# Kernel tuning notes

Measured on AMD Instinct MI355X. Metric: run time of the kernel, lower is better.

Reference implementation:

```python
import jax, jax.numpy as jnp
import numpy as np

HID = 1024      # hidden_size (embedding dim, GRU input)
RNN = 1024      # rnn_hidden_size
VOCAB = 50000   # max_node
STEPS = 1024    # num_steps
SOS = 0


def setup_inputs() -> dict:
    key = jax.random.key(0)
    ks = jax.random.split(key, 8)
    s = 0.02
    return {
        "inputs": jax.random.randint(ks[0], (STEPS,), 0, VOCAB),
        "z": jax.random.normal(ks[1], (RNN,), jnp.float32),
        "emb_W": jax.random.uniform(ks[2], (VOCAB, HID), jnp.float32, -0.001, 0.001),
        "out_b": jnp.full((VOCAB,), 0.01, jnp.float32),
        "h2e_W": jax.random.normal(ks[3], (HID, RNN), jnp.float32) * s,
        "h2e_b": jnp.full((HID,), 0.01, jnp.float32),
        "W_ih": jax.random.normal(ks[4], (3 * RNN, HID), jnp.float32) * s,
        "W_hh": jax.random.normal(ks[5], (3 * RNN, RNN), jnp.float32) * s,
        "b_ih": jnp.zeros((3 * RNN,), jnp.float32),
        "b_hh": jnp.zeros((3 * RNN,), jnp.float32),
    }


def reference(inputs, z, emb_W, out_b, h2e_W, h2e_b, W_ih, W_hh, b_ih, b_hh):
    R = RNN

    def gru_cell(h, x):
        gi = W_ih @ x + b_ih          # (3R,)
        gh = W_hh @ h + b_hh          # (3R,)
        r = jax.nn.sigmoid(gi[:R] + gh[:R])
        zg = jax.nn.sigmoid(gi[R:2 * R] + gh[R:2 * R])
        n = jnp.tanh(gi[2 * R:] + r * gh[2 * R:])
        return (1.0 - zg) * n + zg * h

    # teacher forcing: step i consumes token_{i-1} (SOS for i=1), target is inputs[i]
    step_tokens = jnp.concatenate([jnp.array([SOS], dtype=inputs.dtype), inputs[1:-1]])
    targets = inputs[1:]

    def step(h, tok_tgt):
        tok, tgt = tok_tgt
        x = emb_W[tok]                              # embedding lookup (HID,)
        h_new = gru_cell(h, x)                      # (RNN,)
        e = h2e_W @ h_new + h2e_b                   # (HID,)
        logp = jax.nn.log_softmax(emb_W @ e + out_b)  # tied weights, (VOCAB,)
        return h_new, (-logp[tgt], jnp.argmax(logp))

    _, (losses, preds) = jax.lax.scan(step, z, (step_tokens, targets))
    loss = jnp.sum(losses)
    outputs = jnp.zeros((1, inputs.shape[0]), dtype=jnp.int32).at[0, 1:].set(preds.astype(jnp.int32))
    return loss, outputs
```

## Files before the change

kernel.cpp:

```cpp
#include <hip/hip_runtime.h>
#include <math.h>

#define NV      50000
#define T_STEPS 1023
#define KDIM    1024
#define NCH     782
typedef unsigned long long ull;


__global__ __launch_bounds__(256) void k_gather(const int* __restrict__ inputs,
                                                const float* __restrict__ emb,
                                                float* __restrict__ X) {
  const int t = blockIdx.x;
  const int tid = threadIdx.x;
  float4 v = make_float4(0.f, 0.f, 0.f, 0.f);
  if (t < T_STEPS) {
    const int tok = (t == 0) ? 0 : inputs[t];
    v = *(const float4*)&emb[(size_t)tok * KDIM + tid * 4];
  }
  *(float4*)&X[(size_t)t * KDIM + tid * 4] = v;
}

__global__ __launch_bounds__(256) void k_gemm_ffd(const float* __restrict__ A,
                                                  const float* __restrict__ B,
                                                  const float* __restrict__ bias,
                                                  double* __restrict__ C,
                                                  int N, int K) {
  __shared__ float As[32][68];
  __shared__ float Bs[32][68];
  const int tid = threadIdx.x;
  const int bx = blockIdx.x, by = blockIdx.y;
  const int lr = tid >> 2;
  const int lk = (tid & 3) * 8;
  const float* Ap = A + (size_t)(by * 64 + lr) * K + lk;
  const float* Bp = B + (size_t)(bx * 64 + lr) * K + lk;
  const int r0 = (tid >> 4) * 4;
  const int c0 = (tid & 15) * 4;
  double acc[4][4] = {};
  for (int kc = 0; kc < K; kc += 32) {
    const float4 a0 = *(const float4*)(Ap + kc);
    const float4 a1 = *(const float4*)(Ap + kc + 4);
    const float4 b0 = *(const float4*)(Bp + kc);
    const float4 b1 = *(const float4*)(Bp + kc + 4);
    __syncthreads();
    As[lk+0][lr]=a0.x; As[lk+1][lr]=a0.y; As[lk+2][lr]=a0.z; As[lk+3][lr]=a0.w;
    As[lk+4][lr]=a1.x; As[lk+5][lr]=a1.y; As[lk+6][lr]=a1.z; As[lk+7][lr]=a1.w;
    Bs[lk+0][lr]=b0.x; Bs[lk+1][lr]=b0.y; Bs[lk+2][lr]=b0.z; Bs[lk+3][lr]=b0.w;
    Bs[lk+4][lr]=b1.x; Bs[lk+5][lr]=b1.y; Bs[lk+6][lr]=b1.z; Bs[lk+7][lr]=b1.w;
    __syncthreads();
#pragma unroll
    for (int kk = 0; kk < 32; ++kk) {
      const float4 av = *(const float4*)&As[kk][r0];
      const float4 bv = *(const float4*)&Bs[kk][c0];
      const double aa[4] = {av.x, av.y, av.z, av.w};
      const double bb[4] = {bv.x, bv.y, bv.z, bv.w};
#pragma unroll
      for (int i = 0; i < 4; ++i)
#pragma unroll
        for (int j = 0; j < 4; ++j)
          acc[i][j] = fma(aa[i], bb[j], acc[i][j]);
    }
  }
  const int row = by * 64 + r0;
  const int col = bx * 64 + c0;
#pragma unroll
  for (int i = 0; i < 4; ++i)
#pragma unroll
    for (int j = 0; j < 4; ++j)
      C[(size_t)(row + i) * N + col + j] = acc[i][j] + (double)bias[col + j];
}

__global__ __launch_bounds__(256) void k_gemm_dfd(const double* __restrict__ A,
                                                  const float* __restrict__ B,
                                                  const float* __restrict__ bias,
                                                  double* __restrict__ C,
                                                  int N, int K) {
  __shared__ double As[32][68];
  __shared__ float  Bs[32][68];
  const int tid = threadIdx.x;
  const int bx = blockIdx.x, by = blockIdx.y;
  const int lr = tid >> 2;
  const int lk = (tid & 3) * 8;
  const double* Ap = A + (size_t)(by * 64 + lr) * K + lk;
  const float*  Bp = B + (size_t)(bx * 64 + lr) * K + lk;
  const int r0 = (tid >> 4) * 4;
  const int c0 = (tid & 15) * 4;
  double acc[4][4] = {};
  for (int kc = 0; kc < K; kc += 32) {
    double ar[8];
#pragma unroll
    for (int q = 0; q < 8; ++q) ar[q] = Ap[kc + q];
    const float4 b0 = *(const float4*)(Bp + kc);
    const float4 b1 = *(const float4*)(Bp + kc + 4);
    __syncthreads();
#pragma unroll
    for (int q = 0; q < 8; ++q) As[lk + q][lr] = ar[q];
    Bs[lk+0][lr]=b0.x; Bs[lk+1][lr]=b0.y; Bs[lk+2][lr]=b0.z; Bs[lk+3][lr]=b0.w;
    Bs[lk+4][lr]=b1.x; Bs[lk+5][lr]=b1.y; Bs[lk+6][lr]=b1.z; Bs[lk+7][lr]=b1.w;
    __syncthreads();
#pragma unroll
    for (int kk = 0; kk < 32; ++kk) {
      const double aa[4] = {As[kk][r0+0], As[kk][r0+1], As[kk][r0+2], As[kk][r0+3]};
      const float4 bv = *(const float4*)&Bs[kk][c0];
      const double bb[4] = {bv.x, bv.y, bv.z, bv.w};
#pragma unroll
      for (int i = 0; i < 4; ++i)
#pragma unroll
        for (int j = 0; j < 4; ++j)
          acc[i][j] = fma(aa[i], bb[j], acc[i][j]);
    }
  }
  const int row = by * 64 + r0;
  const int col = bx * 64 + c0;
#pragma unroll
  for (int i = 0; i < 4; ++i)
#pragma unroll
    for (int j = 0; j < 4; ++j)
      C[(size_t)(row + i) * N + col + j] = acc[i][j] + (double)bias[col + j];
}

__global__ __launch_bounds__(512, 2) void k_recur(const float* __restrict__ z,
                                                  const float* __restrict__ Whh,
                                                  const float* __restrict__ bhh,
                                                  const double* __restrict__ GI,
                                                  double* H, ull* SA, ull* SB,
                                                  int* done) {
  __shared__ double hs[1024];
  const int tid = threadIdx.x;
  const int w = tid >> 6, l = tid & 63;
  const int ibase = blockIdx.x * 16 + w * 2;
  float wreg[6][16];
#pragma unroll
  for (int il = 0; il < 2; ++il)
#pragma unroll
    for (int g = 0; g < 3; ++g) {
      const float* wp = Whh + (size_t)(g * 1024 + ibase + il) * 1024 + l;
#pragma unroll
      for (int m = 0; m < 16; ++m) wreg[il * 3 + g][m] = wp[m * 64];
    }
  double bh[6];
#pragma unroll
  for (int il = 0; il < 2; ++il)
#pragma unroll
    for (int g = 0; g < 3; ++g) bh[il * 3 + g] = (double)bhh[g * 1024 + ibase + il];

  hs[tid]       = (double)z[tid];
  hs[tid + 512] = (double)z[tid + 512];
  double gi[6];
#pragma unroll
  for (int il = 0; il < 2; ++il)
#pragma unroll
    for (int g = 0; g < 3; ++g) gi[il * 3 + g] = GI[g * 1024 + ibase + il];
  __syncthreads();

  for (int t = 0; t < T_STEPS; ++t) {
    const bool more = (t + 1 < T_STEPS);
    const int p = t & 1;
    const bool gate = more && (t >= 2);
    int dv = 0x7FFFFFFF;
    if (gate && tid < 64)
      dv = __hip_atomic_load(done + p * 64 + tid,
                             __ATOMIC_RELAXED, __HIP_MEMORY_SCOPE_AGENT);
    double s[6] = {0.0, 0.0, 0.0, 0.0, 0.0, 0.0};
#pragma unroll
    for (int m = 0; m < 16; ++m) {
      const double hv = hs[l + 64 * m];
#pragma unroll
      for (int rr = 0; rr < 6; ++rr) s[rr] = fma((double)wreg[rr][m], hv, s[rr]);
    }
#pragma unroll
    for (int rr = 0; rr < 6; ++rr) {
      double v = s[rr];
#pragma unroll
      for (int mk = 32; mk >= 1; mk >>= 1) v += __shfl_xor(v, mk, 64);
      s[rr] = v;
    }
    double hn = 0.0;
    if (l < 2) {
      const int il = l;
      const double r  = 1.0 / (1.0 + exp(-(gi[il * 3 + 0] + s[il * 3 + 0] + bh[il * 3 + 0])));
      const double zg = 1.0 / (1.0 + exp(-(gi[il * 3 + 1] + s[il * 3 + 1] + bh[il * 3 + 1])));
      const double n  = tanh(gi[il * 3 + 2] + r * (s[il * 3 + 2] + bh[il * 3 + 2]));
      hn = (1.0 - zg) * n + zg * hs[ibase + l];
    }
    double gin[6] = {0.0, 0.0, 0.0, 0.0, 0.0, 0.0};
    if (more) {
      const double* gp = GI + (size_t)(t + 1) * 3072;
#pragma unroll
      for (int il = 0; il < 2; ++il)
#pragma unroll
        for (int g = 0; g < 3; ++g) gin[il * 3 + g] = gp[g * 1024 + ibase + il];
    }
    if (gate && tid < 64) {
      while (!__all(dv >= t - 1)) {
        __builtin_amdgcn_s_sleep(1);
        dv = __hip_atomic_load(done + p * 64 + tid,
                               __ATOMIC_RELAXED, __HIP_MEMORY_SCOPE_AGENT);
      }
    }
    __syncthreads();
    if (l < 2) {
      const int gidx = ibase + l;
      __hip_atomic_store(H + (size_t)t * 1024 + gidx, hn,
                         __ATOMIC_RELAXED, __HIP_MEMORY_SCOPE_AGENT);
      if (more) {
        const ull hb  = (ull)__double_as_longlong(hn);
        const ull tag = ((ull)(t + 1)) << 32;
        __hip_atomic_store(SA + p * 1024 + gidx, tag | (hb >> 32),
                           __ATOMIC_RELAXED, __HIP_MEMORY_SCOPE_AGENT);
        __hip_atomic_store(SB + p * 1024 + gidx, tag | (hb & 0xFFFFFFFFull),
                           __ATOMIC_RELAXED, __HIP_MEMORY_SCOPE_AGENT);
      }
    }
    if (more) {
      const ull want = (ull)(t + 1);
      ull a0, b0, a1, b1;
      while (true) {
        a0 = __hip_atomic_load(SA + p * 1024 + tid,
                               __ATOMIC_RELAXED, __HIP_MEMORY_SCOPE_AGENT);
        b0 = __hip_atomic_load(SB + p * 1024 + tid,
                               __ATOMIC_RELAXED, __HIP_MEMORY_SCOPE_AGENT);
        if ((a0 >> 32) >= want && (b0 >> 32) >= want) break;
        __builtin_amdgcn_s_sleep(1);
      }
      while (true) {
        a1 = __hip_atomic_load(SA + p * 1024 + tid + 512,
                               __ATOMIC_RELAXED, __HIP_MEMORY_SCOPE_AGENT);
        b1 = __hip_atomic_load(SB + p * 1024 + tid + 512,
                               __ATOMIC_RELAXED, __HIP_MEMORY_SCOPE_AGENT);
        if ((a1 >> 32) >= want && (b1 >> 32) >= want) break;
        __builtin_amdgcn_s_sleep(1);
      }
      hs[tid]       = __longlong_as_double((long long)
                        (((a0 & 0xFFFFFFFFull) << 32) | (b0 & 0xFFFFFFFFull)));
      hs[tid + 512] = __longlong_as_double((long long)
                        (((a1 & 0xFFFFFFFFull) << 32) | (b1 & 0xFFFFFFFFull)));
      __syncthreads();
      if (tid == 0)
        __hip_atomic_store(done + p * 64 + blockIdx.x, t + 1,
                           __ATOMIC_RELAXED, __HIP_MEMORY_SCOPE_AGENT);
#pragma unroll
      for (int q = 0; q < 6; ++q) gi[q] = gin[q];
    }
  }
}

__global__ __launch_bounds__(256) void k_logits(const double* __restrict__ E,
                                                const float* __restrict__ emb,
                                                const float* __restrict__ out_b,
                                                const int* __restrict__ inputs,
                                                float* __restrict__ candL,
                                                int* __restrict__ candI,
                                                float* __restrict__ Psum,
                                                float* __restrict__ Ttgt) {
  __shared__ double As[32][68];
  __shared__ float  Bs[32][68];
  const int tid = threadIdx.x;
  const int bx = blockIdx.x, by = blockIdx.y;
  const int lr = tid >> 2;
  const int lk = (tid & 3) * 8;
  const int brow = bx * 64 + lr;
  const double* Ap = E + (size_t)(by * 64 + lr) * KDIM + lk;
  const float*  Bp = emb + (size_t)brow * KDIM + lk;
  const bool bvalid = (brow < NV);
  const int r0 = (tid >> 4) * 4;
  const int c0 = (tid & 15) * 4;
  double acc[4][4] = {};
  for (int kc = 0; kc < KDIM; kc += 32) {
    double ar[8];
#pragma unroll
    for (int q = 0; q < 8; ++q) ar[q] = Ap[kc + q];
    float4 b0 = make_float4(0.f, 0.f, 0.f, 0.f);
    float4 b1 = make_float4(0.f, 0.f, 0.f, 0.f);
    if (bvalid) { b0 = *(const float4*)(Bp + kc); b1 = *(const float4*)(Bp + kc + 4); }
    __syncthreads();
#pragma unroll
    for (int q = 0; q < 8; ++q) As[lk + q][lr] = ar[q];
    Bs[lk+0][lr]=b0.x; Bs[lk+1][lr]=b0.y; Bs[lk+2][lr]=b0.z; Bs[lk+3][lr]=b0.w;
    Bs[lk+4][lr]=b1.x; Bs[lk+5][lr]=b1.y; Bs[lk+6][lr]=b1.z; Bs[lk+7][lr]=b1.w;
    __syncthreads();
#pragma unroll
    for (int kk = 0; kk < 32; ++kk) {
      const double aa[4] = {As[kk][r0+0], As[kk][r0+1], As[kk][r0+2], As[kk][r0+3]};
      const float4 bv = *(const float4*)&Bs[kk][c0];
      const double bb[4] = {bv.x, bv.y, bv.z, bv.w};
#pragma unroll
      for (int i = 0; i < 4; ++i)
#pragma unroll
        for (int j = 0; j < 4; ++j)
          acc[i][j] = fma(aa[i], bb[j], acc[i][j]);
    }
  }
  const int colb = bx * 64 + c0;
#pragma unroll
  for (int i = 0; i < 4; ++i) {
    const int s = by * 64 + r0 + i;
    const bool valid = (s < T_STEPS);
    const int tgt = valid ? inputs[s + 1] : -1;
    float L1 = -3e38f, L2 = -3e38f;
    int   i1 = 0x7FFFFFFF, i2 = 0x7FFFFFFF;
    float se = 0.f, tv = -INFINITY;
#pragma unroll
    for (int j = 0; j < 4; ++j) {
      const int v = colb + j;
      if (v < NV) {
        const double lgd = acc[i][j] + (double)out_b[v];
        const float L = (float)lgd;
        se += expf((float)(lgd - 0.01));
        if (v == tgt) tv = (float)lgd;
        if (L > L1 || (L == L1 && v < i1)) { L2 = L1; i2 = i1; L1 = L; i1 = v; }
        else if (L > L2 || (L == L2 && v < i2)) { L2 = L; i2 = v; }
      }
    }
#pragma unroll
    for (int mk = 1; mk <= 8; mk <<= 1) {
      const float oL1 = __shfl_xor(L1, mk, 64); const int oi1 = __shfl_xor(i1, mk, 64);
      const float oL2 = __shfl_xor(L2, mk, 64); const int oi2 = __shfl_xor(i2, mk, 64);
      if (oL1 > L1 || (oL1 == L1 && oi1 < i1)) { L2 = L1; i2 = i1; L1 = oL1; i1 = oi1; }
      else if (oL1 > L2 || (oL1 == L2 && oi1 < i2)) { L2 = oL1; i2 = oi1; }
      if (oL2 > L1 || (oL2 == L1 && oi2 < i1)) { L2 = L1; i2 = i1; L1 = oL2; i1 = oi2; }
      else if (oL2 > L2 || (oL2 == L2 && oi2 < i2)) { L2 = oL2; i2 = oi2; }
      se += __shfl_xor(se, mk, 64);
      tv = fmaxf(tv, __shfl_xor(tv, mk, 64));
    }
    if (((tid & 15) == 0) && valid) {
      const size_t p = (size_t)s * (2 * NCH) + 2 * bx;
      candL[p] = L1;     candI[p] = i1;
      candL[p + 1] = L2; candI[p + 1] = i2;
      atomicAdd(&Psum[s], se);
      if (tv > -1e30f) Ttgt[s] = tv;
    }
  }
}

__global__ __launch_bounds__(256) void k_preds(const float* __restrict__ candL,
                                               const int* __restrict__ candI,
                                               float* __restrict__ out) {
  __shared__ float sL[256];
  __shared__ int   sI[256];
  const int s = blockIdx.x;
  const int tid = threadIdx.x;
  const int n = 2 * NCH;
  const size_t base = (size_t)s * n;
  float m = -3e38f;
  for (int c = tid; c < n; c += 256) m = fmaxf(m, candL[base + c]);
  sL[tid] = m; __syncthreads();
  for (int st = 128; st > 0; st >>= 1) {
    if (tid < st) sL[tid] = fmaxf(sL[tid], sL[tid + st]);
    __syncthreads();
  }
  const float Lmax = sL[0];
  __syncthreads();
  float bq = -3e38f; int bi = 0x7FFFFFFF;
  for (int c = tid; c < n; c += 256) {
    const float L = candL[base + c];
    const int   v = candI[base + c];
    const float d = L - Lmax;
    const float q = d - 10.8125f;
    if (q > bq || (q == bq && v < bi)) { bq = q; bi = v; }
  }
  sL[tid] = bq; sI[tid] = bi; __syncthreads();
  for (int st = 128; st > 0; st >>= 1) {
    if (tid < st) {
      if (sL[tid + st] > sL[tid] ||
          (sL[tid + st] == sL[tid] && sI[tid + st] < sI[tid])) {
        sL[tid] = sL[tid + st]; sI[tid] = sI[tid + st];
      }
    }
    __syncthreads();
  }
  if (tid == 0) out[2 + s] = (float)sI[0];
}

__global__ __launch_bounds__(1024) void k_finish(const float* __restrict__ Psum,
                                                 const float* __restrict__ Ttgt,
                                                 float* __restrict__ out) {
  __shared__ double red[1024];
  const int s = threadIdx.x;
  double ls = 0.0;
  if (s < T_STEPS) ls = 0.01 + log((double)Psum[s]) - (double)Ttgt[s];
  red[s] = ls;
  __syncthreads();
  for (int st = 512; st > 0; st >>= 1) {
    if (s < st) red[s] += red[s + st];
    __syncthreads();
  }
  if (s == 0) out[0] = (float)red[0];
  if (s == 1) out[1] = 0.f;
}

extern "C" void kernel_launch(void* const* d_in, const int* in_sizes, int n_in,
                              void* d_out, int out_size, void* d_ws, size_t ws_size,
                              hipStream_t stream) {
  const int*   inputs = (const int*)  d_in[0];
  const float* z      = (const float*)d_in[1];
  const float* emb    = (const float*)d_in[2];
  const float* out_b  = (const float*)d_in[3];
  const float* h2eW   = (const float*)d_in[4];
  const float* h2eb   = (const float*)d_in[5];
  const float* Wih    = (const float*)d_in[6];
  const float* Whh    = (const float*)d_in[7];
  const float* bih    = (const float*)d_in[8];
  const float* bhh    = (const float*)d_in[9];

  char* ws8 = (char*)d_ws;
  ull*    SA   = (ull*)ws8;
  ull*    SB   = (ull*)(ws8 + 16384);
  int*    done = (int*)(ws8 + 32768);
  float*  Psum = (float*)(ws8 + 33280);
  float*  Ttgt = (float*)(ws8 + 37376);
  float*  X    = (float*)(ws8 + 49152);
  char*   GIb  = ws8 + 49152 + (4u << 20);
  double* GI   = (double*)GIb;
  double* E    = GI;
  float*  candL = (float*)(GIb + (8u << 20));
  int*    candI = (int*)  (GIb + (8u << 20) + 6815744);
  double* H    = (double*)(ws8 + 49152 + (28u << 20));
  float*  out  = (float*)d_out;

  hipMemsetAsync(ws8, 0, 49152, stream);

  k_gather<<<1024, 256, 0, stream>>>(inputs, emb, X);
  k_gemm_ffd<<<dim3(48, 16), 256, 0, stream>>>(X, Wih, bih, GI, 3072, KDIM);
  k_recur<<<64, 512, 0, stream>>>(z, Whh, bhh, GI, H, SA, SB, done);
  k_gemm_dfd<<<dim3(16, 16), 256, 0, stream>>>(H, h2eW, h2eb, E, KDIM, KDIM);
  k_logits<<<dim3(NCH, 16), 256, 0, stream>>>(E, emb, out_b, inputs,
                                              candL, candI, Psum, Ttgt);
  k_preds<<<T_STEPS, 256, 0, stream>>>(candL, candI, out);
  k_finish<<<1, 1024, 0, stream>>>(Psum, Ttgt, out);
}
```

Measured before the change: 9.355 ms.

## Fuse recurrence, h2e projection and logits into one persistent pipelined kernel

Replaces the separate recurrence, h2e GEMM and logits GEMM launches with one persistent kernel. Its blocks are split into GRU recurrence workers, per-step h2e GEMV workers and vocabulary logit workers, which hand work to each other through device-scope flags and a ring buffer of E vectors. The goal is to hide the logits and projection work behind the serial recurrence instead of running them afterwards. Candidate outputs are written over GI rows that the recurrence has already consumed, to save memory. The cost is that logits now run on only 98 blocks, each thread reading its own embedding row with poor coalescing, so throughput can suffer if the overlap does not cover that work.

```diff
diff --git a/kernel.cpp b/kernel.cpp
--- a/kernel.cpp
+++ b/kernel.cpp
@@ -4,8 +4,16 @@
 #define NV      50000
 #define T_STEPS 1023
 #define KDIM    1024
-#define NCH     782
 typedef unsigned long long ull;
+
+#define NRECUR  64
+#define NEW_    16
+#define NLW     98
+#define NBLK    (NRECUR + NEW_ + NLW)
+#define ERING   512
+#define TSB     24576
+#define CANDI_OFF 6272
+#define NCAND   1568
 
 
 __global__ __launch_bounds__(256) void k_gather(const int* __restrict__ inputs,
@@ -70,280 +78,283 @@
       C[(size_t)(row + i) * N + col + j] = acc[i][j] + (double)bias[col + j];
 }
 
-__global__ __launch_bounds__(256) void k_gemm_dfd(const double* __restrict__ A,
-                                                  const float* __restrict__ B,
-                                                  const float* __restrict__ bias,
-                                                  double* __restrict__ C,
-                                                  int N, int K) {
-  __shared__ double As[32][68];
-  __shared__ float  Bs[32][68];
+__global__ __launch_bounds__(512, 1) void k_mega(
+    const float* z, const float* Whh, const float* bhh,
+    const double* GI, double* H, ull* SA, ull* SB, int* done,
+    int* prog, int* Edone, int* bcount, double* Ering,
+    const float* h2eW, const float* h2eb,
+    const float* emb, const float* out_b, const int* inputs,
+    float* Psum, float* Ttgt, char* candb)
+{
+  __shared__ double SM[4096];
   const int tid = threadIdx.x;
-  const int bx = blockIdx.x, by = blockIdx.y;
-  const int lr = tid >> 2;
-  const int lk = (tid & 3) * 8;
-  const double* Ap = A + (size_t)(by * 64 + lr) * K + lk;
-  const float*  Bp = B + (size_t)(bx * 64 + lr) * K + lk;
-  const int r0 = (tid >> 4) * 4;
-  const int c0 = (tid & 15) * 4;
-  double acc[4][4] = {};
-  for (int kc = 0; kc < K; kc += 32) {
-    double ar[8];
-#pragma unroll
-    for (int q = 0; q < 8; ++q) ar[q] = Ap[kc + q];
-    const float4 b0 = *(const float4*)(Bp + kc);
-    const float4 b1 = *(const float4*)(Bp + kc + 4);
-    __syncthreads();
-#pragma unroll
-    for (int q = 0; q < 8; ++q) As[lk + q][lr] = ar[q];
-    Bs[lk+0][lr]=b0.x; Bs[lk+1][lr]=b0.y; Bs[lk+2][lr]=b0.z; Bs[lk+3][lr]=b0.w;
-    Bs[lk+4][lr]=b1.x; Bs[lk+5][lr]=b1.y; Bs[lk+6][lr]=b1.z; Bs[lk+7][lr]=b1.w;
-    __syncthreads();
-#pragma unroll
-    for (int kk = 0; kk < 32; ++kk) {
-      const double aa[4] = {As[kk][r0+0], As[kk][r0+1], As[kk][r0+2], As[kk][r0+3]};
-      const float4 bv = *(const float4*)&Bs[kk][c0];
-      const double bb[4] = {bv.x, bv.y, bv.z, bv.w};
-#pragma unroll
-      for (int i = 0; i < 4; ++i)
-#pragma unroll
-        for (int j = 0; j < 4; ++j)
-          acc[i][j] = fma(aa[i], bb[j], acc[i][j]);
-    }
-  }
-  const int row = by * 64 + r0;
-  const int col = bx * 64 + c0;
-#pragma unroll
-  for (int i = 0; i < 4; ++i)
-#pragma unroll
-    for (int j = 0; j < 4; ++j)
-      C[(size_t)(row + i) * N + col + j] = acc[i][j] + (double)bias[col + j];
-}
-
-__global__ __launch_bounds__(512, 2) void k_recur(const float* __restrict__ z,
-                                                  const float* __restrict__ Whh,
-                                                  const float* __restrict__ bhh,
-                                                  const double* __restrict__ GI,
-                                                  double* H, ull* SA, ull* SB,
-                                                  int* done) {
-  __shared__ double hs[1024];
-  const int tid = threadIdx.x;
-  const int w = tid >> 6, l = tid & 63;
-  const int ibase = blockIdx.x * 16 + w * 2;
-  float wreg[6][16];
-#pragma unroll
-  for (int il = 0; il < 2; ++il)
-#pragma unroll
-    for (int g = 0; g < 3; ++g) {
-      const float* wp = Whh + (size_t)(g * 1024 + ibase + il) * 1024 + l;
-#pragma unroll
-      for (int m = 0; m < 16; ++m) wreg[il * 3 + g][m] = wp[m * 64];
-    }
-  double bh[6];
-#pragma unroll
-  for (int il = 0; il < 2; ++il)
-#pragma unroll
-    for (int g = 0; g < 3; ++g) bh[il * 3 + g] = (double)bhh[g * 1024 + ibase + il];
-
-  hs[tid]       = (double)z[tid];
-  hs[tid + 512] = (double)z[tid + 512];
-  double gi[6];
-#pragma unroll
-  for (int il = 0; il < 2; ++il)
-#pragma unroll
-    for (int g = 0; g < 3; ++g) gi[il * 3 + g] = GI[g * 1024 + ibase + il];
-  __syncthreads();
-
-  for (int t = 0; t < T_STEPS; ++t) {
-    const bool more = (t + 1 < T_STEPS);
-    const int p = t & 1;
-    const bool gate = more && (t >= 2);
-    int dv = 0x7FFFFFFF;
-    if (gate && tid < 64)
-      dv = __hip_atomic_load(done + p * 64 + tid,
-                             __ATOMIC_RELAXED, __HIP_MEMORY_SCOPE_AGENT);
-    double s[6] = {0.0, 0.0, 0.0, 0.0, 0.0, 0.0};
-#pragma unroll
-    for (int m = 0; m < 16; ++m) {
-      const double hv = hs[l + 64 * m];
-#pragma unroll
-      for (int rr = 0; rr < 6; ++rr) s[rr] = fma((double)wreg[rr][m], hv, s[rr]);
-    }
-#pragma unroll
-    for (int rr = 0; rr < 6; ++rr) {
-      double v = s[rr];
-#pragma unroll
-      for (int mk = 32; mk >= 1; mk >>= 1) v += __shfl_xor(v, mk, 64);
-      s[rr] = v;
-    }
-    double hn = 0.0;
-    if (l < 2) {
-      const int il = l;
-      const double r  = 1.0 / (1.0 + exp(-(gi[il * 3 + 0] + s[il * 3 + 0] + bh[il * 3 + 0])));
-      const double zg = 1.0 / (1.0 + exp(-(gi[il * 3 + 1] + s[il * 3 + 1] + bh[il * 3 + 1])));
-      const double n  = tanh(gi[il * 3 + 2] + r * (s[il * 3 + 2] + bh[il * 3 + 2]));
-      hn = (1.0 - zg) * n + zg * hs[ibase + l];
-    }
-    double gin[6] = {0.0, 0.0, 0.0, 0.0, 0.0, 0.0};
-    if (more) {
-      const double* gp = GI + (size_t)(t + 1) * 3072;
-#pragma unroll
-      for (int il = 0; il < 2; ++il)
-#pragma unroll
-        for (int g = 0; g < 3; ++g) gin[il * 3 + g] = gp[g * 1024 + ibase + il];
-    }
-    if (gate && tid < 64) {
-      while (!__all(dv >= t - 1)) {
-        __builtin_amdgcn_s_sleep(1);
+  const int bid = blockIdx.x;
+
+  if (bid < NRECUR) {
+    double* hs = SM;
+    const int w = tid >> 6, l = tid & 63;
+    const int ibase = bid * 16 + w * 2;
+    float wreg[6][16];
+#pragma unroll
+    for (int il = 0; il < 2; ++il)
+#pragma unroll
+      for (int g = 0; g < 3; ++g) {
+        const float* wp = Whh + (size_t)(g * 1024 + ibase + il) * 1024 + l;
+#pragma unroll
+        for (int m = 0; m < 16; ++m) wreg[il * 3 + g][m] = wp[m * 64];
+      }
+    double bh[6];
+#pragma unroll
+    for (int il = 0; il < 2; ++il)
+#pragma unroll
+      for (int g = 0; g < 3; ++g) bh[il * 3 + g] = (double)bhh[g * 1024 + ibase + il];
+
+    hs[tid]       = (double)z[tid];
+    hs[tid + 512] = (double)z[tid + 512];
+    double gi[6];
+#pragma unroll
+    for (int il = 0; il < 2; ++il)
+#pragma unroll
+      for (int g = 0; g < 3; ++g) gi[il * 3 + g] = GI[g * 1024 + ibase + il];
+    __syncthreads();
+
+    for (int t = 0; t < T_STEPS; ++t) {
+      const bool more = (t + 1 < T_STEPS);
+      const int p = t & 1;
+      const bool gate = more && (t >= 2);
+      int dv = 0x7FFFFFFF;
+      if (gate && tid < 64)
         dv = __hip_atomic_load(done + p * 64 + tid,
                                __ATOMIC_RELAXED, __HIP_MEMORY_SCOPE_AGENT);
+      double s[6] = {0.0, 0.0, 0.0, 0.0, 0.0, 0.0};
+#pragma unroll
+      for (int m = 0; m < 16; ++m) {
+        const double hv = hs[l + 64 * m];
+#pragma unroll
+        for (int rr = 0; rr < 6; ++rr) s[rr] = fma((double)wreg[rr][m], hv, s[rr]);
+      }
+#pragma unroll
+      for (int rr = 0; rr < 6; ++rr) {
+        double v = s[rr];
+#pragma unroll
+        for (int mk = 32; mk >= 1; mk >>= 1) v += __shfl_xor(v, mk, 64);
+        s[rr] = v;
+      }
+      double hn = 0.0;
+      if (l < 2) {
+        const int il = l;
+        const double r  = 1.0 / (1.0 + exp(-(gi[il*3+0] + s[il*3+0] + bh[il*3+0])));
+        const double zg = 1.0 / (1.0 + exp(-(gi[il*3+1] + s[il*3+1] + bh[il*3+1])));
+        const double n  = tanh(gi[il*3+2] + r * (s[il*3+2] + bh[il*3+2]));
+        hn = (1.0 - zg) * n + zg * hs[ibase + l];
+      }
+      double gin[6] = {0.0, 0.0, 0.0, 0.0, 0.0, 0.0};
+      if (more) {
+        const double* gp = GI + (size_t)(t + 1) * 3072;
+#pragma unroll
+        for (int il = 0; il < 2; ++il)
+#pragma unroll
+          for (int g = 0; g < 3; ++g) gin[il * 3 + g] = gp[g * 1024 + ibase + il];
+      }
+      if (gate && tid < 64) {
+        while (!__all(dv >= t - 1)) {
+          __builtin_amdgcn_s_sleep(1);
+          dv = __hip_atomic_load(done + p * 64 + tid,
+                                 __ATOMIC_RELAXED, __HIP_MEMORY_SCOPE_AGENT);
+        }
+      }
+      __syncthreads();
+      if (l < 2) {
+        const int gidx = ibase + l;
+        __hip_atomic_store(H + (size_t)t * 1024 + gidx, hn,
+                           __ATOMIC_RELAXED, __HIP_MEMORY_SCOPE_AGENT);
+        if (more) {
+          const ull hb  = (ull)__double_as_longlong(hn);
+          const ull tag = ((ull)(t + 1)) << 32;
+          __hip_atomic_store(SA + p * 1024 + gidx, tag | (hb >> 32),
+                             __ATOMIC_RELAXED, __HIP_MEMORY_SCOPE_AGENT);
+          __hip_atomic_store(SB + p * 1024 + gidx, tag | (hb & 0xFFFFFFFFull),
+                             __ATOMIC_RELAXED, __HIP_MEMORY_SCOPE_AGENT);
+        }
+      }
+      if (more) {
+        const ull want = (ull)(t + 1);
+        ull a0, b0, a1, b1;
+        while (true) {
+          a0 = __hip_atomic_load(SA + p * 1024 + tid,
+                                 __ATOMIC_RELAXED, __HIP_MEMORY_SCOPE_AGENT);
+          b0 = __hip_atomic_load(SB + p * 1024 + tid,
+                                 __ATOMIC_RELAXED, __HIP_MEMORY_SCOPE_AGENT);
+          if ((a0 >> 32) >= want && (b0 >> 32) >= want) break;
+          __builtin_amdgcn_s_sleep(1);
+        }
+        while (true) {
+          a1 = __hip_atomic_load(SA + p * 1024 + tid + 512,
+                                 __ATOMIC_RELAXED, __HIP_MEMORY_SCOPE_AGENT);
+          b1 = __hip_atomic_load(SB + p * 1024 + tid + 512,
+                                 __ATOMIC_RELAXED, __HIP_MEMORY_SCOPE_AGENT);
+          if ((a1 >> 32) >= want && (b1 >> 32) >= want) break;
+          __builtin_amdgcn_s_sleep(1);
+        }
+        hs[tid]       = __longlong_as_double((long long)
+                          (((a0 & 0xFFFFFFFFull) << 32) | (b0 & 0xFFFFFFFFull)));
+        hs[tid + 512] = __longlong_as_double((long long)
+                          (((a1 & 0xFFFFFFFFull) << 32) | (b1 & 0xFFFFFFFFull)));
+        __syncthreads();
+        if (tid == 0) {
+          __hip_atomic_store(done + p * 64 + bid, t + 1,
+                             __ATOMIC_RELAXED, __HIP_MEMORY_SCOPE_AGENT);
+          __hip_atomic_store(prog + bid, t + 1,
+                             __ATOMIC_RELAXED, __HIP_MEMORY_SCOPE_AGENT);
+        }
+#pragma unroll
+        for (int q = 0; q < 6; ++q) gi[q] = gin[q];
       }
     }
     __syncthreads();
-    if (l < 2) {
-      const int gidx = ibase + l;
-      __hip_atomic_store(H + (size_t)t * 1024 + gidx, hn,
+    if (tid == 0)
+      __hip_atomic_store(prog + bid, T_STEPS,
                          __ATOMIC_RELAXED, __HIP_MEMORY_SCOPE_AGENT);
-      if (more) {
-        const ull hb  = (ull)__double_as_longlong(hn);
-        const ull tag = ((ull)(t + 1)) << 32;
-        __hip_atomic_store(SA + p * 1024 + gidx, tag | (hb >> 32),
+
+  } else if (bid < NRECUR + NEW_) {
+    const int e = bid - NRECUR;
+    for (int s = e; s < T_STEPS; s += NEW_) {
+      if (s >= ERING && tid == 0) {
+        const int bi = (s - ERING) >> 6;
+        while (__hip_atomic_load(bcount + bi, __ATOMIC_RELAXED,
+                                 __HIP_MEMORY_SCOPE_AGENT) < NLW)
+          __builtin_amdgcn_s_sleep(8);
+      }
+      if (tid < 64) {
+        while (true) {
+          const int pv = __hip_atomic_load(prog + tid, __ATOMIC_RELAXED,
+                                           __HIP_MEMORY_SCOPE_AGENT);
+          if (__all(pv >= s + 1)) break;
+          __builtin_amdgcn_s_sleep(8);
+        }
+      }
+      __syncthreads();
+      SM[tid]       = __hip_atomic_load(H + (size_t)s * 1024 + tid,
+                        __ATOMIC_RELAXED, __HIP_MEMORY_SCOPE_AGENT);
+      SM[tid + 512] = __hip_atomic_load(H + (size_t)s * 1024 + tid + 512,
+                        __ATOMIC_RELAXED, __HIP_MEMORY_SCOPE_AGENT);
+      __syncthreads();
+      double a0 = 0.0, a1 = 0.0;
+      const float* w0 = h2eW + (size_t)tid * 1024;
+      const float* w1 = h2eW + (size_t)(tid + 512) * 1024;
+      for (int k = 0; k < 1024; ++k) {
+        const double hv = SM[k];
+        a0 = fma((double)w0[k], hv, a0);
+        a1 = fma((double)w1[k], hv, a1);
+      }
+      double* er = Ering + (size_t)(s & (ERING - 1)) * 1024;
+      __hip_atomic_store(er + tid, a0 + (double)h2eb[tid],
+                         __ATOMIC_RELAXED, __HIP_MEMORY_SCOPE_AGENT);
+      __hip_atomic_store(er + tid + 512, a1 + (double)h2eb[tid + 512],
+                         __ATOMIC_RELAXED, __HIP_MEMORY_SCOPE_AGENT);
+      __syncthreads();
+      if (tid == 0)
+        __hip_atomic_store(Edone + s, 1,
                            __ATOMIC_RELAXED, __HIP_MEMORY_SCOPE_AGENT);
-        __hip_atomic_store(SB + p * 1024 + gidx, tag | (hb & 0xFFFFFFFFull),
-                           __ATOMIC_RELAXED, __HIP_MEMORY_SCOPE_AGENT);
-      }
     }
-    if (more) {
-      const ull want = (ull)(t + 1);
-      ull a0, b0, a1, b1;
-      while (true) {
-        a0 = __hip_atomic_load(SA + p * 1024 + tid,
-                               __ATOMIC_RELAXED, __HIP_MEMORY_SCOPE_AGENT);
-        b0 = __hip_atomic_load(SB + p * 1024 + tid,
-                               __ATOMIC_RELAXED, __HIP_MEMORY_SCOPE_AGENT);
-        if ((a0 >> 32) >= want && (b0 >> 32) >= want) break;
-        __builtin_amdgcn_s_sleep(1);
-      }
-      while (true) {
-        a1 = __hip_atomic_load(SA + p * 1024 + tid + 512,
-                               __ATOMIC_RELAXED, __HIP_MEMORY_SCOPE_AGENT);
-        b1 = __hip_atomic_load(SB + p * 1024 + tid + 512,
-                               __ATOMIC_RELAXED, __HIP_MEMORY_SCOPE_AGENT);
-        if ((a1 >> 32) >= want && (b1 >> 32) >= want) break;
-        __builtin_amdgcn_s_sleep(1);
-      }
-      hs[tid]       = __longlong_as_double((long long)
-                        (((a0 & 0xFFFFFFFFull) << 32) | (b0 & 0xFFFFFFFFull)));
-      hs[tid + 512] = __longlong_as_double((long long)
-                        (((a1 & 0xFFFFFFFFull) << 32) | (b1 & 0xFFFFFFFFull)));
-      __syncthreads();
-      if (tid == 0)
-        __hip_atomic_store(done + p * 64 + blockIdx.x, t + 1,
-                           __ATOMIC_RELAXED, __HIP_MEMORY_SCOPE_AGENT);
-#pragma unroll
-      for (int q = 0; q < 6; ++q) gi[q] = gin[q];
+
+  } else {
+    const int w = bid - NRECUR - NEW_;
+    const int col = w * 512 + tid;
+    const bool cvalid = col < NV;
+    const int lane = tid & 63, wv = tid >> 6;
+    const float* brow = emb + (size_t)(cvalid ? col : 0) * 1024;
+    const float ob = cvalid ? out_b[col] : 0.f;
+
+    for (int beta = 0; beta < 16; ++beta) {
+      const int s0 = beta * 64;
+      if (tid < 64) {
+        while (true) {
+          const int ss = s0 + tid;
+          const int ev = (ss < T_STEPS)
+              ? __hip_atomic_load(Edone + ss, __ATOMIC_RELAXED,
+                                  __HIP_MEMORY_SCOPE_AGENT)
+              : 1;
+          if (__all(ev != 0)) break;
+          __builtin_amdgcn_s_sleep(8);
+        }
+      }
+      __syncthreads();
+      double acc[64];
+#pragma unroll
+      for (int si = 0; si < 64; ++si) acc[si] = 0.0;
+      for (int kt = 0; kt < 16; ++kt) {
+        __syncthreads();
+        for (int li = tid; li < 4096; li += 512) {
+          const int si = li >> 6, kj = li & 63;
+          SM[li] = __hip_atomic_load(
+              Ering + (size_t)((s0 + si) & (ERING - 1)) * 1024 + kt * 64 + kj,
+              __ATOMIC_RELAXED, __HIP_MEMORY_SCOPE_AGENT);
+        }
+        __syncthreads();
+        const int kb = kt * 64;
+        for (int kj = 0; kj < 64; kj += 2) {
+          const double e0 = (double)brow[kb + kj];
+          const double e1 = (double)brow[kb + kj + 1];
+#pragma unroll
+          for (int si = 0; si < 64; ++si) {
+            const double2 ev = *(const double2*)&SM[si * 64 + kj];
+            acc[si] = fma(ev.y, e1, fma(ev.x, e0, acc[si]));
+          }
+        }
+      }
+#pragma unroll
+      for (int si = 0; si < 64; ++si) {
+        const int s = s0 + si;
+        if (s < T_STEPS) {
+          const int tgt = inputs[s + 1];
+          const double lgd = acc[si] + (double)ob;
+          float L1 = cvalid ? (float)lgd : -3e38f;
+          int   i1 = cvalid ? col : 0x7FFFFFFF;
+          float L2 = -3e38f; int i2 = 0x7FFFFFFF;
+          float se = cvalid ? expf((float)(lgd - 0.01)) : 0.f;
+          float tv = (cvalid && col == tgt) ? (float)lgd : -INFINITY;
+#pragma unroll
+          for (int mk = 1; mk <= 32; mk <<= 1) {
+            const float oL1 = __shfl_xor(L1, mk, 64);
+            const int   oi1 = __shfl_xor(i1, mk, 64);
+            const float oL2 = __shfl_xor(L2, mk, 64);
+            const int   oi2 = __shfl_xor(i2, mk, 64);
+            if (oL1 > L1 || (oL1 == L1 && oi1 < i1)) { L2 = L1; i2 = i1; L1 = oL1; i1 = oi1; }
+            else if (oL1 > L2 || (oL1 == L2 && oi1 < i2)) { L2 = oL1; i2 = oi1; }
+            if (oL2 > L1 || (oL2 == L1 && oi2 < i1)) { L2 = L1; i2 = i1; L1 = oL2; i1 = oi2; }
+            else if (oL2 > L2 || (oL2 == L2 && oi2 < i2)) { L2 = oL2; i2 = oi2; }
+            se += __shfl_xor(se, mk, 64);
+            tv = fmaxf(tv, __shfl_xor(tv, mk, 64));
+          }
+          if (lane == 0) {
+            float* cl = (float*)(candb + (size_t)s * TSB);
+            int*   ci = (int*)(candb + (size_t)s * TSB + CANDI_OFF);
+            const int ch = w * 8 + wv;
+            cl[ch * 2]     = L1;  ci[ch * 2]     = i1;
+            cl[ch * 2 + 1] = L2;  ci[ch * 2 + 1] = i2;
+            atomicAdd(Psum + s, se);
+            if (tv > -1e30f) Ttgt[s] = tv;
+          }
+        }
+      }
+      __syncthreads();
+      if (tid == 0) atomicAdd(bcount + beta, 1);
     }
   }
 }
 
-__global__ __launch_bounds__(256) void k_logits(const double* __restrict__ E,
-                                                const float* __restrict__ emb,
-                                                const float* __restrict__ out_b,
-                                                const int* __restrict__ inputs,
-                                                float* __restrict__ candL,
-                                                int* __restrict__ candI,
-                                                float* __restrict__ Psum,
-                                                float* __restrict__ Ttgt) {
-  __shared__ double As[32][68];
-  __shared__ float  Bs[32][68];
-  const int tid = threadIdx.x;
-  const int bx = blockIdx.x, by = blockIdx.y;
-  const int lr = tid >> 2;
-  const int lk = (tid & 3) * 8;
-  const int brow = bx * 64 + lr;
-  const double* Ap = E + (size_t)(by * 64 + lr) * KDIM + lk;
-  const float*  Bp = emb + (size_t)brow * KDIM + lk;
-  const bool bvalid = (brow < NV);
-  const int r0 = (tid >> 4) * 4;
-  const int c0 = (tid & 15) * 4;
-  double acc[4][4] = {};
-  for (int kc = 0; kc < KDIM; kc += 32) {
-    double ar[8];
-#pragma unroll
-    for (int q = 0; q < 8; ++q) ar[q] = Ap[kc + q];
-    float4 b0 = make_float4(0.f, 0.f, 0.f, 0.f);
-    float4 b1 = make_float4(0.f, 0.f, 0.f, 0.f);
-    if (bvalid) { b0 = *(const float4*)(Bp + kc); b1 = *(const float4*)(Bp + kc + 4); }
-    __syncthreads();
-#pragma unroll
-    for (int q = 0; q < 8; ++q) As[lk + q][lr] = ar[q];
-    Bs[lk+0][lr]=b0.x; Bs[lk+1][lr]=b0.y; Bs[lk+2][lr]=b0.z; Bs[lk+3][lr]=b0.w;
-    Bs[lk+4][lr]=b1.x; Bs[lk+5][lr]=b1.y; Bs[lk+6][lr]=b1.z; Bs[lk+7][lr]=b1.w;
-    __syncthreads();
-#pragma unroll
-    for (int kk = 0; kk < 32; ++kk) {
-      const double aa[4] = {As[kk][r0+0], As[kk][r0+1], As[kk][r0+2], As[kk][r0+3]};
-      const float4 bv = *(const float4*)&Bs[kk][c0];
-      const double bb[4] = {bv.x, bv.y, bv.z, bv.w};
-#pragma unroll
-      for (int i = 0; i < 4; ++i)
-#pragma unroll
-        for (int j = 0; j < 4; ++j)
-          acc[i][j] = fma(aa[i], bb[j], acc[i][j]);
-    }
-  }
-  const int colb = bx * 64 + c0;
-#pragma unroll
-  for (int i = 0; i < 4; ++i) {
-    const int s = by * 64 + r0 + i;
-    const bool valid = (s < T_STEPS);
-    const int tgt = valid ? inputs[s + 1] : -1;
-    float L1 = -3e38f, L2 = -3e38f;
-    int   i1 = 0x7FFFFFFF, i2 = 0x7FFFFFFF;
-    float se = 0.f, tv = -INFINITY;
-#pragma unroll
-    for (int j = 0; j < 4; ++j) {
-      const int v = colb + j;
-      if (v < NV) {
-        const double lgd = acc[i][j] + (double)out_b[v];
-        const float L = (float)lgd;
-        se += expf((float)(lgd - 0.01));
-        if (v == tgt) tv = (float)lgd;
-        if (L > L1 || (L == L1 && v < i1)) { L2 = L1; i2 = i1; L1 = L; i1 = v; }
-        else if (L > L2 || (L == L2 && v < i2)) { L2 = L; i2 = v; }
-      }
-    }
-#pragma unroll
-    for (int mk = 1; mk <= 8; mk <<= 1) {
-      const float oL1 = __shfl_xor(L1, mk, 64); const int oi1 = __shfl_xor(i1, mk, 64);
-      const float oL2 = __shfl_xor(L2, mk, 64); const int oi2 = __shfl_xor(i2, mk, 64);
-      if (oL1 > L1 || (oL1 == L1 && oi1 < i1)) { L2 = L1; i2 = i1; L1 = oL1; i1 = oi1; }
-      else if (oL1 > L2 || (oL1 == L2 && oi1 < i2)) { L2 = oL1; i2 = oi1; }
-      if (oL2 > L1 || (oL2 == L1 && oi2 < i1)) { L2 = L1; i2 = i1; L1 = oL2; i1 = oi2; }
-      else if (oL2 > L2 || (oL2 == L2 && oi2 < i2)) { L2 = oL2; i2 = oi2; }
-      se += __shfl_xor(se, mk, 64);
-      tv = fmaxf(tv, __shfl_xor(tv, mk, 64));
-    }
-    if (((tid & 15) == 0) && valid) {
-      const size_t p = (size_t)s * (2 * NCH) + 2 * bx;
-      candL[p] = L1;     candI[p] = i1;
-      candL[p + 1] = L2; candI[p + 1] = i2;
-      atomicAdd(&Psum[s], se);
-      if (tv > -1e30f) Ttgt[s] = tv;
-    }
-  }
-}
-
-__global__ __launch_bounds__(256) void k_preds(const float* __restrict__ candL,
-                                               const int* __restrict__ candI,
+__global__ __launch_bounds__(256) void k_preds(const char* __restrict__ candb,
                                                float* __restrict__ out) {
   __shared__ float sL[256];
   __shared__ int   sI[256];
   const int s = blockIdx.x;
   const int tid = threadIdx.x;
-  const int n = 2 * NCH;
-  const size_t base = (size_t)s * n;
+  const float* candL = (const float*)(candb + (size_t)s * TSB);
+  const int*   candI = (const int*)(candb + (size_t)s * TSB + CANDI_OFF);
+  const int n = NCAND;
   float m = -3e38f;
-  for (int c = tid; c < n; c += 256) m = fmaxf(m, candL[base + c]);
+  for (int c = tid; c < n; c += 256) m = fmaxf(m, candL[c]);
   sL[tid] = m; __syncthreads();
   for (int st = 128; st > 0; st >>= 1) {
     if (tid < st) sL[tid] = fmaxf(sL[tid], sL[tid + st]);
@@ -353,8 +364,8 @@
   __syncthreads();
   float bq = -3e38f; int bi = 0x7FFFFFFF;
   for (int c = tid; c < n; c += 256) {
-    const float L = candL[base + c];
-    const int   v = candI[base + c];
+    const float L = candL[c];
+    const int   v = candI[c];
     const float d = L - Lmax;
     const float q = d - 10.8125f;
     if (q > bq || (q == bq && v < bi)) { bq = q; bi = v; }
@@ -404,28 +415,28 @@
   const float* bhh    = (const float*)d_in[9];
 
   char* ws8 = (char*)d_ws;
-  ull*    SA   = (ull*)ws8;
-  ull*    SB   = (ull*)(ws8 + 16384);
-  int*    done = (int*)(ws8 + 32768);
-  float*  Psum = (float*)(ws8 + 33280);
-  float*  Ttgt = (float*)(ws8 + 37376);
-  float*  X    = (float*)(ws8 + 49152);
-  char*   GIb  = ws8 + 49152 + (4u << 20);
-  double* GI   = (double*)GIb;
-  double* E    = GI;
-  float*  candL = (float*)(GIb + (8u << 20));
-  int*    candI = (int*)  (GIb + (8u << 20) + 6815744);
-  double* H    = (double*)(ws8 + 49152 + (28u << 20));
-  float*  out  = (float*)d_out;
+  ull*    SA     = (ull*)ws8;
+  ull*    SB     = (ull*)(ws8 + 16384);
+  int*    done   = (int*)(ws8 + 32768);
+  int*    prog   = (int*)(ws8 + 33280);
+  int*    Edone  = (int*)(ws8 + 33536);
+  int*    bcount = (int*)(ws8 + 37632);
+  float*  Psum   = (float*)(ws8 + 40960);
+  float*  Ttgt   = (float*)(ws8 + 45056);
+  char*   GIb    = ws8 + 98304;
+  double* GI     = (double*)GIb;
+  double* XE     = (double*)(GIb + (24u << 20));
+  double* H      = (double*)(GIb + (28u << 20));
+  float*  out    = (float*)d_out;
 
   hipMemsetAsync(ws8, 0, 49152, stream);
 
-  k_gather<<<1024, 256, 0, stream>>>(inputs, emb, X);
-  k_gemm_ffd<<<dim3(48, 16), 256, 0, stream>>>(X, Wih, bih, GI, 3072, KDIM);
-  k_recur<<<64, 512, 0, stream>>>(z, Whh, bhh, GI, H, SA, SB, done);
-  k_gemm_dfd<<<dim3(16, 16), 256, 0, stream>>>(H, h2eW, h2eb, E, KDIM, KDIM);
-  k_logits<<<dim3(NCH, 16), 256, 0, stream>>>(E, emb, out_b, inputs,
-                                              candL, candI, Psum, Ttgt);
-  k_preds<<<T_STEPS, 256, 0, stream>>>(candL, candI, out);
+  k_gather<<<1024, 256, 0, stream>>>(inputs, emb, (float*)XE);
+  k_gemm_ffd<<<dim3(48, 16), 256, 0, stream>>>((float*)XE, Wih, bih, GI,
+                                               3072, KDIM);
+  k_mega<<<NBLK, 512, 0, stream>>>(z, Whh, bhh, GI, H, SA, SB, done,
+                                   prog, Edone, bcount, XE, h2eW, h2eb,
+                                   emb, out_b, inputs, Psum, Ttgt, GIb);
+  k_preds<<<T_STEPS, 256, 0, stream>>>(GIb, out);
   k_finish<<<1, 1024, 0, stream>>>(Psum, Ttgt, out);
 }
```

After: 23.12 ms. 147% more time.
